# Kernel optimization log

Measured on AMD Instinct MI355X. Metric: run time of the kernel, lower is better.

Reference implementation:

```python
import jax, jax.numpy as jnp
import numpy as np

D_K = 512  # module-level global used for the scale factor


def setup_inputs() -> dict:
    key = jax.random.key(0)
    kq, kk, kv, km = jax.random.split(key, 4)
    B, H, L = 4, 8, 1024
    Q = jax.random.normal(kq, (B, H, L, D_K), dtype=jnp.float32)
    K = jax.random.normal(kk, (B, H, L, D_K), dtype=jnp.float32)
    V = jax.random.normal(kv, (B, H, L, D_K), dtype=jnp.float32)
    attn_mask = jax.random.randint(km, (B, H, L, L), 0, 2).astype(jnp.bool_)
    return {"Q": Q, "K": K, "V": V, "attn_mask": attn_mask}


def reference(Q, K, V, attn_mask):
    scale = 1.0 / np.sqrt(D_K).astype(np.float32)
    # [B,H,Lq,Lk]
    scores = jnp.einsum('bhqd,bhkd->bhqk', Q, K) * scale
    scores = jnp.where(attn_mask, jnp.float32(-1e9), scores)
    attn = jax.nn.softmax(scores, axis=-1)
    context = jnp.einsum('bhqk,bhkd->bhqd', attn, V)
    return (context, attn)
```

## Files before the change

kernel.cpp:

```cpp
#include <hip/hip_runtime.h>
#include <hip/hip_bf16.h>

constexpr int BH  = 32;
constexpr int LQ  = 1024;
constexpr int DK  = 512;
constexpr float SCALE = 0.04419417382415922f;

using short8 = __attribute__((ext_vector_type(8))) short;
using f32x4  = __attribute__((ext_vector_type(4))) float;

__device__ __forceinline__ unsigned short cvt_bf16(float x) {
  unsigned int u = __builtin_bit_cast(unsigned int, x);
  u += 0x7FFFu + ((u >> 16) & 1u);
  return (unsigned short)(u >> 16);
}
__device__ __forceinline__ float bf2f(unsigned short s) {
  return __builtin_bit_cast(float, (unsigned int)s << 16);
}
__device__ __forceinline__ unsigned int pkbf(float lo, float hi) {
  unsigned int r;
  asm("v_cvt_pk_bf16_f32 %0, %1, %2" : "=v"(r) : "v"(lo), "v"(hi));
  return r;
}

__device__ __forceinline__ void lds_load16(const void* g, void* l) {
  __builtin_amdgcn_global_load_lds(
      (const __attribute__((address_space(1))) unsigned int*)g,
      (__attribute__((address_space(3))) unsigned int*)l, 16, 0, 0);
}

__global__ __launch_bounds__(256) void cvt2_f32_bf16(
    const float* __restrict__ s0, const float* __restrict__ s1,
    unsigned short* __restrict__ d0, unsigned short* __restrict__ d1, int n8) {
  const float* src = blockIdx.y ? s1 : s0;
  unsigned short* dst = blockIdx.y ? d1 : d0;
  int i = blockIdx.x * 256 + threadIdx.x;
  const int stride = gridDim.x * 256;
  for (; i < n8; i += stride) {
    float4 a = ((const float4*)src)[(size_t)i * 2];
    float4 b = ((const float4*)src)[(size_t)i * 2 + 1];
    unsigned int w[4] __attribute__((aligned(16)));
    w[0] = pkbf(a.x, a.y); w[1] = pkbf(a.z, a.w);
    w[2] = pkbf(b.x, b.y); w[3] = pkbf(b.z, b.w);
    ((uint4*)dst)[i] = *(uint4*)w;
  }
}

__global__ __launch_bounds__(512) void qk_v4_kernel(
    const unsigned short* __restrict__ A, const unsigned short* __restrict__ B,
    const int* __restrict__ mask, unsigned short* __restrict__ P,
    float* __restrict__ partials) {
  __shared__ __attribute__((aligned(16))) unsigned short smem[24576];

  int flat = blockIdx.x + 8 * (blockIdx.y + 4 * blockIdx.z);
  flat = (flat % 8) * 128 + flat / 8;
  const int bx = flat % 8;
  const int by = (flat / 8) % 4;
  const int bh = flat / 32;

  const int t = threadIdx.x;
  const int lane = t & 63, wave = t >> 6;
  const int wr = wave >> 1;
  const int wc = wave & 1;
  const int fr = lane & 15, fq = lane >> 4;
  const int m0 = by * 256, n0 = bx * 128;

  const char* Ab = (const char*)A + ((size_t)bh * LQ + m0) * 1024;
  const char* Bb = (const char*)B + ((size_t)bh * LQ + n0) * 1024;

  unsigned int orv = 0;
  {
    const unsigned int* mw = (const unsigned int*)mask;
    #pragma unroll
    for (int i = 0; i < 64; ++i) orv |= mw[i];
  }
  const bool byteMode = (orv > 1u);

  f32x4 acc[4][4];
  #pragma unroll
  for (int i = 0; i < 4; ++i)
    #pragma unroll
    for (int j = 0; j < 4; ++j) acc[i][j] = (f32x4){0.f, 0.f, 0.f, 0.f};

  char* const AsB = (char*)smem;
  char* const BsB = (char*)smem + 32768;

  for (int kt = 0; kt < 8; ++kt) {
    const int kb = kt * 128;
    __syncthreads();
    #pragma unroll
    for (int i = 0; i < 4; ++i) {
      const int p  = i * 8192 + t * 16;
      const int r  = p >> 7;
      const int ch = (p >> 4) & 7;
      lds_load16(Ab + (size_t)r * 1024 + kb + ((ch ^ (r & 7)) << 4),
                 AsB + i * 8192 + wave * 1024);
    }
    #pragma unroll
    for (int i = 0; i < 2; ++i) {
      const int p  = i * 8192 + t * 16;
      const int r  = p >> 7;
      const int ch = (p >> 4) & 7;
      lds_load16(Bb + (size_t)r * 1024 + kb + ((ch ^ (r & 7)) << 4),
                 BsB + i * 8192 + wave * 1024);
    }
    __syncthreads();

    #pragma unroll
    for (int kk = 0; kk < 2; ++kk) {
      short8 a[4], b[4];
      #pragma unroll
      for (int mi = 0; mi < 4; ++mi) {
        const int r  = wr * 64 + mi * 16 + fr;
        const int ch = (kk * 4 + fq) ^ (r & 7);
        a[mi] = *(const short8*)(AsB + r * 128 + ch * 16);
      }
      #pragma unroll
      for (int ni = 0; ni < 4; ++ni) {
        const int r  = wc * 64 + ni * 16 + fr;
        const int ch = (kk * 4 + fq) ^ (r & 7);
        b[ni] = *(const short8*)(BsB + r * 128 + ch * 16);
      }
      #pragma unroll
      for (int mi = 0; mi < 4; ++mi)
        #pragma unroll
        for (int ni = 0; ni < 4; ++ni)
          acc[mi][ni] = __builtin_amdgcn_mfma_f32_16x16x32_bf16(a[mi], b[ni], acc[mi][ni], 0, 0, 0);
    }
  }

  unsigned short* Cs = smem;
  const size_t pbase = (size_t)bh * LQ * LQ;
  #pragma unroll
  for (int h = 0; h < 2; ++h) {
    __syncthreads();
    if ((wr >> 1) == h) {
      #pragma unroll
      for (int mi = 0; mi < 4; ++mi)
        #pragma unroll
        for (int ni = 0; ni < 4; ++ni) {
          const int col = wc * 64 + ni * 16 + fr;
          #pragma unroll
          for (int r = 0; r < 4; ++r) {
            const int rloc = (wr & 1) * 64 + mi * 16 + fq * 4 + r;
            Cs[rloc * 136 + col] = cvt_bf16(__expf(acc[mi][ni][r] * SCALE));
          }
        }
    }
    __syncthreads();
    const int rl = t >> 4;
    const int cl = (t & 15) * 8;
    #pragma unroll
    for (int rb = 0; rb < 4; ++rb) {
      const int rloc = rb * 32 + rl;
      const int rg   = m0 + h * 128 + rloc;
      const size_t gidx = pbase + (size_t)rg * LQ + (n0 + cl);
      short8 sv = *(const short8*)&Cs[rloc * 136 + cl];
      bool mk[8];
      if (byteMode) {
        const unsigned char* mb = (const unsigned char*)mask + gidx;
        uint2 w = *(const uint2*)mb;
        #pragma unroll
        for (int j = 0; j < 4; ++j) mk[j]     = ((w.x >> (8 * j)) & 255u) != 0u;
        #pragma unroll
        for (int j = 0; j < 4; ++j) mk[4 + j] = ((w.y >> (8 * j)) & 255u) != 0u;
      } else {
        int4 w0 = *(const int4*)(mask + gidx);
        int4 w1 = *(const int4*)(mask + gidx + 4);
        mk[0] = w0.x != 0; mk[1] = w0.y != 0; mk[2] = w0.z != 0; mk[3] = w0.w != 0;
        mk[4] = w1.x != 0; mk[5] = w1.y != 0; mk[6] = w1.z != 0; mk[7] = w1.w != 0;
      }
      unsigned short out[8] __attribute__((aligned(16)));
      float s = 0.f;
      #pragma unroll
      for (int j = 0; j < 8; ++j) {
        unsigned short v = mk[j] ? (unsigned short)0 : (unsigned short)sv[j];
        out[j] = v;
        s += bf2f(v);
      }
      *(short8*)(P + gidx) = *(short8*)out;
      s += __shfl_xor(s, 1); s += __shfl_xor(s, 2);
      s += __shfl_xor(s, 4); s += __shfl_xor(s, 8);
      if ((t & 15) == 0)
        partials[((size_t)bh * LQ + rg) * 8 + bx] = s;
    }
  }
}

__global__ __launch_bounds__(256) void attn_fin(
    const unsigned short* __restrict__ P, const float* __restrict__ partials,
    float* __restrict__ attn) {
  const int ch = blockIdx.x, rb64 = blockIdx.y, bh = blockIdx.z;
  const int m0 = rb64 * 64;
  __shared__ float invs[64];
  const int t = threadIdx.x;
  if (t < 64) {
    const float* pp = partials + ((size_t)bh * LQ + m0 + t) * 8;
    float s = ((pp[0] + pp[1]) + (pp[2] + pp[3])) + ((pp[4] + pp[5]) + (pp[6] + pp[7]));
    invs[t] = 1.0f / s;
  }
  __syncthreads();
  const size_t pbase = (size_t)bh * LQ * LQ;
  const int c0 = ch * 512;
  #pragma unroll
  for (int rb = 0; rb < 4; ++rb) {
    const int rloc = rb * 16 + (t >> 4);
    const int row  = m0 + rloc;
    const float inv = invs[rloc];
    const size_t base = pbase + (size_t)row * LQ + c0 + (t & 15) * 8;
    #pragma unroll
    for (int j = 0; j < 4; ++j) {
      short8 sv = *(const short8*)(P + base + j * 128);
      float4 o0, o1;
      o0.x = bf2f((unsigned short)sv[0]) * inv;
      o0.y = bf2f((unsigned short)sv[1]) * inv;
      o0.z = bf2f((unsigned short)sv[2]) * inv;
      o0.w = bf2f((unsigned short)sv[3]) * inv;
      o1.x = bf2f((unsigned short)sv[4]) * inv;
      o1.y = bf2f((unsigned short)sv[5]) * inv;
      o1.z = bf2f((unsigned short)sv[6]) * inv;
      o1.w = bf2f((unsigned short)sv[7]) * inv;
      *(float4*)(attn + base + j * 128)     = o0;
      *(float4*)(attn + base + j * 128 + 4) = o1;
    }
  }
}

__global__ __launch_bounds__(256) void pv2_kernel(
    const unsigned short* __restrict__ P, const float* __restrict__ V,
    const float* __restrict__ partials, float* __restrict__ O) {
  __shared__ __attribute__((aligned(16))) unsigned short As[8192];
  __shared__ __attribute__((aligned(16))) unsigned short BsV[128 * 72];
  __shared__ float invsL[128];

  int flat = blockIdx.x + 4 * (blockIdx.y + 8 * blockIdx.z);
  flat = (flat % 8) * 128 + flat / 8;
  const int bx = flat % 4;
  const int by = (flat / 4) % 8;
  const int bh = flat / 32;

  const int t = threadIdx.x;
  const int lane = t & 63, wave = t >> 6;
  const int wr = wave >> 1, wc = wave & 1;
  const int fr = lane & 15, fq = lane >> 4;
  const int m0 = by * 128, n0 = bx * 128;

  if (t < 128) {
    const float* pp = partials + ((size_t)bh * LQ + m0 + t) * 8;
    float s = ((pp[0] + pp[1]) + (pp[2] + pp[3])) + ((pp[4] + pp[5]) + (pp[6] + pp[7]));
    invsL[t] = 1.0f / s;
  }

  const char* Ab  = (const char*)P + ((size_t)bh * LQ + m0) * 2048;
  const float* Vb = V + (size_t)bh * LQ * DK + n0;

  f32x4 acc[4][4];
  #pragma unroll
  for (int i = 0; i < 4; ++i)
    #pragma unroll
    for (int j = 0; j < 4; ++j) acc[i][j] = (f32x4){0.f, 0.f, 0.f, 0.f};

  const int g  = t >> 5;
  const int nl = t & 31;

  float vf[8][4];
  auto V_LOAD = [&](int k0) {
    #pragma unroll
    for (int i = 0; i < 8; ++i) {
      const size_t rb = (size_t)(k0 + 8 * g + i) * DK;
      #pragma unroll
      for (int jn = 0; jn < 4; ++jn)
        vf[i][jn] = Vb[rb + nl + 32 * jn];
    }
  };
  auto V_STORE = [&]() {
    #pragma unroll
    for (int jn = 0; jn < 4; ++jn) {
      const int n = nl + 32 * jn;
      uint2 w0, w1;
      w0.x = pkbf(vf[0][jn], vf[1][jn]); w0.y = pkbf(vf[2][jn], vf[3][jn]);
      w1.x = pkbf(vf[4][jn], vf[5][jn]); w1.y = pkbf(vf[6][jn], vf[7][jn]);
      *(uint2*)((char*)BsV + n * 144 + 16 * g)     = w0;
      *(uint2*)((char*)BsV + n * 144 + 16 * g + 8) = w1;
    }
  };

  V_LOAD(0);

  for (int k0 = 0; k0 < LQ; k0 += 64) {
    __syncthreads();
    V_STORE();
    #pragma unroll
    for (int i = 0; i < 4; ++i) {
      const int p  = i * 4096 + t * 16;
      const int r  = p >> 7;
      const int ch = (p >> 4) & 7;
      const int sw = ((ch ^ (r & 7)) << 4);
      lds_load16(Ab + (size_t)r * 2048 + k0 * 2 + sw, (char*)As + wave * 1024 + i * 4096);
    }
    if (k0 + 64 < LQ) V_LOAD(k0 + 64);
    __syncthreads();

    #pragma unroll
    for (int kk = 0; kk < 2; ++kk) {
      short8 a[4], b[4];
      #pragma unroll
      for (int mi = 0; mi < 4; ++mi) {
        const int r  = wr * 64 + mi * 16 + fr;
        const int ch = (kk * 4 + fq) ^ (r & 7);
        a[mi] = *(const short8*)((const char*)As + r * 128 + ch * 16);
      }
      #pragma unroll
      for (int ni = 0; ni < 4; ++ni) {
        const int r = wc * 64 + ni * 16 + fr;
        b[ni] = *(const short8*)((const char*)BsV + r * 144 + (kk * 4 + fq) * 16);
      }
      #pragma unroll
      for (int mi = 0; mi < 4; ++mi)
        #pragma unroll
        for (int ni = 0; ni < 4; ++ni)
          acc[mi][ni] = __builtin_amdgcn_mfma_f32_16x16x32_bf16(a[mi], b[ni], acc[mi][ni], 0, 0, 0);
    }
  }

  const size_t obase = (size_t)bh * LQ * DK;
  #pragma unroll
  for (int mi = 0; mi < 4; ++mi)
    #pragma unroll
    for (int ni = 0; ni < 4; ++ni) {
      const int col = n0 + wc * 64 + ni * 16 + fr;
      #pragma unroll
      for (int r = 0; r < 4; ++r) {
        const int rloc = wr * 64 + mi * 16 + fq * 4 + r;
        O[obase + (size_t)(m0 + rloc) * DK + col] = acc[mi][ni][r] * invsL[rloc];
      }
    }
}

__global__ __launch_bounds__(256) void qk_mask_kernel(
    const float* __restrict__ Q, const float* __restrict__ Kmat,
    const int* __restrict__ mask, float* __restrict__ S) {
  __shared__ __attribute__((aligned(16))) unsigned short Asf[128][40];
  __shared__ __attribute__((aligned(16))) unsigned short Bsf[128][40];
  const int t = threadIdx.x;
  const int lane = t & 63, wave = t >> 6;
  const int wr = wave >> 1, wc = wave & 1;
  const int fr = lane & 15, fq = lane >> 4;
  const int bh = blockIdx.z;
  const int m0 = blockIdx.y * 128, n0 = blockIdx.x * 128;
  const float* Qb = Q + (size_t)bh * LQ * DK;
  const float* Kb = Kmat + (size_t)bh * LQ * DK;
  unsigned int orv = 0;
  { const unsigned int* mw = (const unsigned int*)mask;
    #pragma unroll
    for (int i = 0; i < 64; ++i) orv |= mw[i]; }
  const bool byteMode = (orv > 1u);
  f32x4 acc[4][4];
  #pragma unroll
  for (int i = 0; i < 4; ++i)
    #pragma unroll
    for (int j = 0; j < 4; ++j) acc[i][j] = (f32x4){0.f,0.f,0.f,0.f};
  const int sr = t >> 1, sc = (t & 1) * 16;
  for (int kd = 0; kd < DK; kd += 32) {
    __syncthreads();
    { const float4* qa = (const float4*)(Qb + (size_t)(m0+sr)*DK + kd + sc);
      float fv[16];
      #pragma unroll
      for (int i = 0; i < 4; ++i) { float4 x = qa[i];
        fv[4*i]=x.x; fv[4*i+1]=x.y; fv[4*i+2]=x.z; fv[4*i+3]=x.w; }
      unsigned short us[16] __attribute__((aligned(16)));
      #pragma unroll
      for (int i = 0; i < 16; ++i) us[i] = cvt_bf16(fv[i]);
      *(short8*)&Asf[sr][sc]   = *(short8*)&us[0];
      *(short8*)&Asf[sr][sc+8] = *(short8*)&us[8]; }
    { const float4* ka = (const float4*)(Kb + (size_t)(n0+sr)*DK + kd + sc);
      float fv[16];
      #pragma unroll
      for (int i = 0; i < 4; ++i) { float4 x = ka[i];
        fv[4*i]=x.x; fv[4*i+1]=x.y; fv[4*i+2]=x.z; fv[4*i+3]=x.w; }
      unsigned short us[16] __attribute__((aligned(16)));
      #pragma unroll
      for (int i = 0; i < 16; ++i) us[i] = cvt_bf16(fv[i]);
      *(short8*)&Bsf[sr][sc]   = *(short8*)&us[0];
      *(short8*)&Bsf[sr][sc+8] = *(short8*)&us[8]; }
    __syncthreads();
    short8 a[4], b[4];
    #pragma unroll
    for (int mi = 0; mi < 4; ++mi) a[mi] = *(const short8*)&Asf[wr*64+mi*16+fr][fq*8];
    #pragma unroll
    for (int ni = 0; ni < 4; ++ni) b[ni] = *(const short8*)&Bsf[wc*64+ni*16+fr][fq*8];
    #pragma unroll
    for (int mi = 0; mi < 4; ++mi)
      #pragma unroll
      for (int ni = 0; ni < 4; ++ni)
        acc[mi][ni] = __builtin_amdgcn_mfma_f32_16x16x32_bf16(a[mi], b[ni], acc[mi][ni], 0, 0, 0);
  }
  const size_t sbase = (size_t)bh * LQ * LQ;
  const unsigned char* mb = (const unsigned char*)mask;
  #pragma unroll
  for (int mi = 0; mi < 4; ++mi)
    #pragma unroll
    for (int ni = 0; ni < 4; ++ni) {
      const int col = n0 + wc*64 + ni*16 + fr;
      #pragma unroll
      for (int r = 0; r < 4; ++r) {
        const int row = m0 + wr*64 + mi*16 + fq*4 + r;
        const size_t idx = sbase + (size_t)row * LQ + col;
        float s = acc[mi][ni][r] * SCALE;
        const bool msk = byteMode ? (mb[idx] != 0) : (mask[idx] != 0);
        S[idx] = msk ? -1e9f : s;
      }
    }
}

__global__ __launch_bounds__(256) void softmax_kernel(float* __restrict__ A) {
  const int row = blockIdx.x;
  float4* rp = (float4*)(A + (size_t)row * LQ);
  const int t = threadIdx.x;
  float4 v = rp[t];
  float m = fmaxf(fmaxf(v.x, v.y), fmaxf(v.z, v.w));
  #pragma unroll
  for (int off = 32; off >= 1; off >>= 1) m = fmaxf(m, __shfl_xor(m, off, 64));
  __shared__ float redm[4];
  const int wv = t >> 6, ln = t & 63;
  if (ln == 0) redm[wv] = m;
  __syncthreads();
  m = fmaxf(fmaxf(redm[0], redm[1]), fmaxf(redm[2], redm[3]));
  float4 e;
  e.x = expf(v.x - m); e.y = expf(v.y - m); e.z = expf(v.z - m); e.w = expf(v.w - m);
  float s = (e.x + e.y) + (e.z + e.w);
  #pragma unroll
  for (int off = 32; off >= 1; off >>= 1) s += __shfl_xor(s, off, 64);
  __shared__ float reds2[4];
  if (ln == 0) reds2[wv] = s;
  __syncthreads();
  s = (reds2[0] + reds2[1]) + (reds2[2] + reds2[3]);
  const float inv = 1.0f / s;
  e.x *= inv; e.y *= inv; e.z *= inv; e.w *= inv;
  rp[t] = e;
}

__global__ __launch_bounds__(256) void pv_kernel(
    const float* __restrict__ P, const float* __restrict__ V, float* __restrict__ O) {
  __shared__ __attribute__((aligned(16))) unsigned short Ps[128][40];
  __shared__ __attribute__((aligned(16))) unsigned short Vtl[128][40];
  const int t = threadIdx.x;
  const int lane = t & 63, wave = t >> 6;
  const int wr = wave >> 1, wc = wave & 1;
  const int fr = lane & 15, fq = lane >> 4;
  const int bh = blockIdx.z;
  const int m0 = blockIdx.y * 128, n0 = blockIdx.x * 128;
  const float* Pb = P + (size_t)bh * LQ * LQ;
  const float* Vb = V + (size_t)bh * LQ * DK;
  f32x4 acc[4][4];
  #pragma unroll
  for (int i = 0; i < 4; ++i)
    #pragma unroll
    for (int j = 0; j < 4; ++j) acc[i][j] = (f32x4){0.f,0.f,0.f,0.f};
  const int sr = t >> 1, sc = (t & 1) * 16;
  const int kk = (t & 15) * 2, nn = (t >> 4) * 8;
  for (int k0 = 0; k0 < LQ; k0 += 32) {
    __syncthreads();
    { const float4* pa = (const float4*)(Pb + (size_t)(m0+sr)*LQ + k0 + sc);
      float fv[16];
      #pragma unroll
      for (int i = 0; i < 4; ++i) { float4 x = pa[i];
        fv[4*i]=x.x; fv[4*i+1]=x.y; fv[4*i+2]=x.z; fv[4*i+3]=x.w; }
      unsigned short us[16] __attribute__((aligned(16)));
      #pragma unroll
      for (int i = 0; i < 16; ++i) us[i] = cvt_bf16(fv[i]);
      *(short8*)&Ps[sr][sc]   = *(short8*)&us[0];
      *(short8*)&Ps[sr][sc+8] = *(short8*)&us[8]; }
    { const float* v0p = Vb + (size_t)(k0+kk)*DK + n0 + nn;
      const float* v1p = v0p + DK;
      float4 a0 = *(const float4*)v0p, a1 = *(const float4*)(v0p+4);
      float4 b0 = *(const float4*)v1p, b1 = *(const float4*)(v1p+4);
      float r0[8] = {a0.x,a0.y,a0.z,a0.w,a1.x,a1.y,a1.z,a1.w};
      float r1[8] = {b0.x,b0.y,b0.z,b0.w,b1.x,b1.y,b1.z,b1.w};
      #pragma unroll
      for (int i = 0; i < 8; ++i) {
        unsigned int pk = (unsigned int)cvt_bf16(r0[i]) | ((unsigned int)cvt_bf16(r1[i]) << 16);
        *(unsigned int*)&Vtl[nn+i][kk] = pk; } }
    __syncthreads();
    short8 a[4], b[4];
    #pragma unroll
    for (int mi = 0; mi < 4; ++mi) a[mi] = *(const short8*)&Ps[wr*64+mi*16+fr][fq*8];
    #pragma unroll
    for (int ni = 0; ni < 4; ++ni) b[ni] = *(const short8*)&Vtl[wc*64+ni*16+fr][fq*8];
    #pragma unroll
    for (int mi = 0; mi < 4; ++mi)
      #pragma unroll
      for (int ni = 0; ni < 4; ++ni)
        acc[mi][ni] = __builtin_amdgcn_mfma_f32_16x16x32_bf16(a[mi], b[ni], acc[mi][ni], 0, 0, 0);
  }
  const size_t obase = (size_t)bh * LQ * DK;
  #pragma unroll
  for (int mi = 0; mi < 4; ++mi)
    #pragma unroll
    for (int ni = 0; ni < 4; ++ni) {
      const int col = n0 + wc*64 + ni*16 + fr;
      #pragma unroll
      for (int r = 0; r < 4; ++r) {
        const int row = m0 + wr*64 + mi*16 + fq*4 + r;
        O[obase + (size_t)row * DK + col] = acc[mi][ni][r];
      }
    }
}

extern "C" void kernel_launch(void* const* d_in, const int* in_sizes, int n_in,
                              void* d_out, int out_size, void* d_ws, size_t ws_size,
                              hipStream_t stream) {
  const float* Q    = (const float*)d_in[0];
  const float* K    = (const float*)d_in[1];
  const float* V    = (const float*)d_in[2];
  const int*   mask = (const int*)d_in[3];

  float* ctx  = (float*)d_out;
  float* attn = ctx + (size_t)BH * LQ * DK;

  const size_t NE = (size_t)BH * LQ * DK;
  const size_t P_BYTES  = (size_t)BH * LQ * LQ * 2;
  const size_t WS_NEED  = P_BYTES + (size_t)BH * LQ * 8 * 4;

  if (ws_size >= WS_NEED) {
    unsigned short* Pp       = (unsigned short*)d_ws;
    float*          partials = (float*)((char*)d_ws + P_BYTES);
    unsigned short* Qb = (unsigned short*)ctx;
    unsigned short* Kb = Qb + NE;

    cvt2_f32_bf16<<<dim3(1024, 2), 256, 0, stream>>>(Q, K, Qb, Kb, (int)(NE / 8));
    qk_v4_kernel<<<dim3(8, 4, BH), 512, 0, stream>>>(Qb, Kb, mask, Pp, partials);
    attn_fin<<<dim3(2, 16, BH), 256, 0, stream>>>(Pp, partials, attn);
    pv2_kernel<<<dim3(4, 8, BH), 256, 0, stream>>>(Pp, V, partials, ctx);
  } else {
    qk_mask_kernel<<<dim3(8, 8, BH), 256, 0, stream>>>(Q, K, mask, attn);
    softmax_kernel<<<dim3(BH * LQ), 256, 0, stream>>>(attn);
    pv_kernel<<<dim3(4, 8, BH), 256, 0, stream>>>(attn, V, ctx);
  }
}
```

Baseline: 218.5 us.

## Fuse fp32-to-bf16 conversion of Q and K into the QK GEMM kernel

```diff
diff --git a/kernel.cpp b/kernel.cpp
--- a/kernel.cpp
+++ b/kernel.cpp
@@ -29,25 +29,8 @@
       (__attribute__((address_space(3))) unsigned int*)l, 16, 0, 0);
 }
 
-__global__ __launch_bounds__(256) void cvt2_f32_bf16(
-    const float* __restrict__ s0, const float* __restrict__ s1,
-    unsigned short* __restrict__ d0, unsigned short* __restrict__ d1, int n8) {
-  const float* src = blockIdx.y ? s1 : s0;
-  unsigned short* dst = blockIdx.y ? d1 : d0;
-  int i = blockIdx.x * 256 + threadIdx.x;
-  const int stride = gridDim.x * 256;
-  for (; i < n8; i += stride) {
-    float4 a = ((const float4*)src)[(size_t)i * 2];
-    float4 b = ((const float4*)src)[(size_t)i * 2 + 1];
-    unsigned int w[4] __attribute__((aligned(16)));
-    w[0] = pkbf(a.x, a.y); w[1] = pkbf(a.z, a.w);
-    w[2] = pkbf(b.x, b.y); w[3] = pkbf(b.z, b.w);
-    ((uint4*)dst)[i] = *(uint4*)w;
-  }
-}
-
-__global__ __launch_bounds__(512) void qk_v4_kernel(
-    const unsigned short* __restrict__ A, const unsigned short* __restrict__ B,
+__global__ __launch_bounds__(512) void qk_v6_kernel(
+    const float* __restrict__ Q, const float* __restrict__ K,
     const int* __restrict__ mask, unsigned short* __restrict__ P,
     float* __restrict__ partials) {
   __shared__ __attribute__((aligned(16))) unsigned short smem[24576];
@@ -65,8 +48,8 @@
   const int fr = lane & 15, fq = lane >> 4;
   const int m0 = by * 256, n0 = bx * 128;
 
-  const char* Ab = (const char*)A + ((size_t)bh * LQ + m0) * 1024;
-  const char* Bb = (const char*)B + ((size_t)bh * LQ + n0) * 1024;
+  const char* Ab = (const char*)(Q + ((size_t)bh * LQ + m0) * DK);
+  const char* Bb = (const char*)(K + ((size_t)bh * LQ + n0) * DK);
 
   unsigned int orv = 0;
   {
@@ -85,7 +68,7 @@
   char* const AsB = (char*)smem;
   char* const BsB = (char*)smem + 32768;
 
-  for (int kt = 0; kt < 8; ++kt) {
+  for (int kt = 0; kt < 16; ++kt) {
     const int kb = kt * 128;
     __syncthreads();
     #pragma unroll
@@ -93,7 +76,7 @@
       const int p  = i * 8192 + t * 16;
       const int r  = p >> 7;
       const int ch = (p >> 4) & 7;
-      lds_load16(Ab + (size_t)r * 1024 + kb + ((ch ^ (r & 7)) << 4),
+      lds_load16(Ab + (size_t)r * 2048 + kb + ((ch ^ (r & 7)) << 4),
                  AsB + i * 8192 + wave * 1024);
     }
     #pragma unroll
@@ -101,32 +84,37 @@
       const int p  = i * 8192 + t * 16;
       const int r  = p >> 7;
       const int ch = (p >> 4) & 7;
-      lds_load16(Bb + (size_t)r * 1024 + kb + ((ch ^ (r & 7)) << 4),
+      lds_load16(Bb + (size_t)r * 2048 + kb + ((ch ^ (r & 7)) << 4),
                  BsB + i * 8192 + wave * 1024);
     }
     __syncthreads();
 
-    #pragma unroll
-    for (int kk = 0; kk < 2; ++kk) {
-      short8 a[4], b[4];
-      #pragma unroll
-      for (int mi = 0; mi < 4; ++mi) {
-        const int r  = wr * 64 + mi * 16 + fr;
-        const int ch = (kk * 4 + fq) ^ (r & 7);
-        a[mi] = *(const short8*)(AsB + r * 128 + ch * 16);
-      }
-      #pragma unroll
-      for (int ni = 0; ni < 4; ++ni) {
-        const int r  = wc * 64 + ni * 16 + fr;
-        const int ch = (kk * 4 + fq) ^ (r & 7);
-        b[ni] = *(const short8*)(BsB + r * 128 + ch * 16);
-      }
-      #pragma unroll
-      for (int mi = 0; mi < 4; ++mi)
-        #pragma unroll
-        for (int ni = 0; ni < 4; ++ni)
-          acc[mi][ni] = __builtin_amdgcn_mfma_f32_16x16x32_bf16(a[mi], b[ni], acc[mi][ni], 0, 0, 0);
-    }
+    short8 a[4], b[4];
+    #pragma unroll
+    for (int mi = 0; mi < 4; ++mi) {
+      const int r = wr * 64 + mi * 16 + fr;
+      const float4 x = *(const float4*)(AsB + r * 128 + (((2 * fq)     ^ (r & 7)) << 4));
+      const float4 y = *(const float4*)(AsB + r * 128 + (((2 * fq + 1) ^ (r & 7)) << 4));
+      unsigned int w[4] __attribute__((aligned(16)));
+      w[0] = pkbf(x.x, x.y); w[1] = pkbf(x.z, x.w);
+      w[2] = pkbf(y.x, y.y); w[3] = pkbf(y.z, y.w);
+      a[mi] = *(short8*)w;
+    }
+    #pragma unroll
+    for (int ni = 0; ni < 4; ++ni) {
+      const int r = wc * 64 + ni * 16 + fr;
+      const float4 x = *(const float4*)(BsB + r * 128 + (((2 * fq)     ^ (r & 7)) << 4));
+      const float4 y = *(const float4*)(BsB + r * 128 + (((2 * fq + 1) ^ (r & 7)) << 4));
+      unsigned int w[4] __attribute__((aligned(16)));
+      w[0] = pkbf(x.x, x.y); w[1] = pkbf(x.z, x.w);
+      w[2] = pkbf(y.x, y.y); w[3] = pkbf(y.z, y.w);
+      b[ni] = *(short8*)w;
+    }
+    #pragma unroll
+    for (int mi = 0; mi < 4; ++mi)
+      #pragma unroll
+      for (int ni = 0; ni < 4; ++ni)
+        acc[mi][ni] = __builtin_amdgcn_mfma_f32_16x16x32_bf16(a[mi], b[ni], acc[mi][ni], 0, 0, 0);
   }
 
   unsigned short* Cs = smem;
@@ -518,18 +506,14 @@
   float* ctx  = (float*)d_out;
   float* attn = ctx + (size_t)BH * LQ * DK;
 
-  const size_t NE = (size_t)BH * LQ * DK;
   const size_t P_BYTES  = (size_t)BH * LQ * LQ * 2;
   const size_t WS_NEED  = P_BYTES + (size_t)BH * LQ * 8 * 4;
 
   if (ws_size >= WS_NEED) {
     unsigned short* Pp       = (unsigned short*)d_ws;
     float*          partials = (float*)((char*)d_ws + P_BYTES);
-    unsigned short* Qb = (unsigned short*)ctx;
-    unsigned short* Kb = Qb + NE;
-
-    cvt2_f32_bf16<<<dim3(1024, 2), 256, 0, stream>>>(Q, K, Qb, Kb, (int)(NE / 8));
-    qk_v4_kernel<<<dim3(8, 4, BH), 512, 0, stream>>>(Qb, Kb, mask, Pp, partials);
+
+    qk_v6_kernel<<<dim3(8, 4, BH), 512, 0, stream>>>(Q, K, mask, Pp, partials);
     attn_fin<<<dim3(2, 16, BH), 256, 0, stream>>>(Pp, partials, attn);
     pv2_kernel<<<dim3(4, 8, BH), 256, 0, stream>>>(Pp, V, partials, ctx);
   } else {
```

Result: slower. 226.6 us (+3.7%).

## Double-buffer QK^T LDS tiles with smaller K-step to overlap loads and MFMA

Applied to the files above, without the earlier changes.

```diff
diff --git a/kernel.cpp b/kernel.cpp
--- a/kernel.cpp
+++ b/kernel.cpp
@@ -46,7 +46,7 @@
   }
 }
 
-__global__ __launch_bounds__(512) void qk_v4_kernel(
+__global__ __launch_bounds__(512) void qk_v7_kernel(
     const unsigned short* __restrict__ A, const unsigned short* __restrict__ B,
     const int* __restrict__ mask, unsigned short* __restrict__ P,
     float* __restrict__ partials) {
@@ -82,51 +82,56 @@
     #pragma unroll
     for (int j = 0; j < 4; ++j) acc[i][j] = (f32x4){0.f, 0.f, 0.f, 0.f};
 
-  char* const AsB = (char*)smem;
-  char* const BsB = (char*)smem + 32768;
-
-  for (int kt = 0; kt < 8; ++kt) {
-    const int kb = kt * 128;
-    __syncthreads();
-    #pragma unroll
-    for (int i = 0; i < 4; ++i) {
-      const int p  = i * 8192 + t * 16;
-      const int r  = p >> 7;
-      const int ch = (p >> 4) & 7;
-      lds_load16(Ab + (size_t)r * 1024 + kb + ((ch ^ (r & 7)) << 4),
-                 AsB + i * 8192 + wave * 1024);
-    }
+  auto STAGE = [&](int kt, int buf) {
+    char* base = (char*)smem + buf * 24576;
+    const int kb = kt * 64;
     #pragma unroll
     for (int i = 0; i < 2; ++i) {
       const int p  = i * 8192 + t * 16;
-      const int r  = p >> 7;
-      const int ch = (p >> 4) & 7;
-      lds_load16(Bb + (size_t)r * 1024 + kb + ((ch ^ (r & 7)) << 4),
-                 BsB + i * 8192 + wave * 1024);
-    }
-    __syncthreads();
-
-    #pragma unroll
-    for (int kk = 0; kk < 2; ++kk) {
-      short8 a[4], b[4];
-      #pragma unroll
-      for (int mi = 0; mi < 4; ++mi) {
-        const int r  = wr * 64 + mi * 16 + fr;
-        const int ch = (kk * 4 + fq) ^ (r & 7);
-        a[mi] = *(const short8*)(AsB + r * 128 + ch * 16);
-      }
-      #pragma unroll
-      for (int ni = 0; ni < 4; ++ni) {
-        const int r  = wc * 64 + ni * 16 + fr;
-        const int ch = (kk * 4 + fq) ^ (r & 7);
-        b[ni] = *(const short8*)(BsB + r * 128 + ch * 16);
-      }
-      #pragma unroll
-      for (int mi = 0; mi < 4; ++mi)
-        #pragma unroll
-        for (int ni = 0; ni < 4; ++ni)
-          acc[mi][ni] = __builtin_amdgcn_mfma_f32_16x16x32_bf16(a[mi], b[ni], acc[mi][ni], 0, 0, 0);
-    }
+      const int r  = p >> 6;
+      const int ch = (p >> 4) & 3;
+      lds_load16(Ab + (size_t)r * 1024 + kb + ((ch ^ (r & 3)) << 4),
+                 base + i * 8192 + wave * 1024);
+    }
+    {
+      const int p  = t * 16;
+      const int r  = p >> 6;
+      const int ch = (p >> 4) & 3;
+      lds_load16(Bb + (size_t)r * 1024 + kb + ((ch ^ (r & 3)) << 4),
+                 base + 16384 + wave * 1024);
+    }
+  };
+  auto COMPUTE = [&](int buf) {
+    const char* As = (const char*)smem + buf * 24576;
+    const char* Bs = As + 16384;
+    short8 a[4], b[4];
+    #pragma unroll
+    for (int mi = 0; mi < 4; ++mi) {
+      const int r  = wr * 64 + mi * 16 + fr;
+      const int ch = fq ^ (r & 3);
+      a[mi] = *(const short8*)(As + r * 64 + ch * 16);
+    }
+    #pragma unroll
+    for (int ni = 0; ni < 4; ++ni) {
+      const int r  = wc * 64 + ni * 16 + fr;
+      const int ch = fq ^ (r & 3);
+      b[ni] = *(const short8*)(Bs + r * 64 + ch * 16);
+    }
+    #pragma unroll
+    for (int mi = 0; mi < 4; ++mi)
+      #pragma unroll
+      for (int ni = 0; ni < 4; ++ni)
+        acc[mi][ni] = __builtin_amdgcn_mfma_f32_16x16x32_bf16(a[mi], b[ni], acc[mi][ni], 0, 0, 0);
+  };
+
+  STAGE(0, 0);
+  __syncthreads();
+  int cur = 0;
+  for (int kt = 0; kt < 16; ++kt) {
+    if (kt < 15) STAGE(kt + 1, cur ^ 1);
+    COMPUTE(cur);
+    __syncthreads();
+    cur ^= 1;
   }
 
   unsigned short* Cs = smem;
@@ -529,7 +534,7 @@
     unsigned short* Kb = Qb + NE;
 
     cvt2_f32_bf16<<<dim3(1024, 2), 256, 0, stream>>>(Q, K, Qb, Kb, (int)(NE / 8));
-    qk_v4_kernel<<<dim3(8, 4, BH), 512, 0, stream>>>(Qb, Kb, mask, Pp, partials);
+    qk_v7_kernel<<<dim3(8, 4, BH), 512, 0, stream>>>(Qb, Kb, mask, Pp, partials);
     attn_fin<<<dim3(2, 16, BH), 256, 0, stream>>>(Pp, partials, attn);
     pv2_kernel<<<dim3(4, 8, BH), 256, 0, stream>>>(Pp, V, partials, ctx);
   } else {
```

After: 222.1 us. No clear change (+1.6%).
